# Kernel tuning notes

Measured on AMD Instinct MI355X. Metric: run time of the kernel, lower is better.

The kernel has to match this reference:

```python
import jax, jax.numpy as jnp
import numpy as np

DIM, H, DH = 1024, 16, 64
SCALE = 1.0 / np.sqrt(DH)


def setup_inputs() -> dict:
    key = jax.random.key(0)
    ks = jax.random.split(key, 16)
    B, S = 2, 2048
    glorot = jax.nn.initializers.glorot_uniform()
    def qkv(k):
        return glorot(k, (DIM, H, DH), jnp.float32)
    inp = {
        "x": jax.random.normal(ks[0], (B, S, DIM), jnp.float32),
        "layer_idx": 3,
        "lambda_param": jnp.full((1,), 0.8, jnp.float32),
    }
    for i, br in enumerate(["1", "2"]):
        base = 1 + i * 4
        inp[f"Wq{br}"] = qkv(ks[base])
        inp[f"Wk{br}"] = qkv(ks[base + 1])
        inp[f"Wv{br}"] = qkv(ks[base + 2])
        inp[f"Wo{br}"] = glorot(ks[base + 3], (H, DH, DIM), jnp.float32).reshape(H, DH, DIM)
        inp[f"bq{br}"] = jnp.zeros((H, DH), jnp.float32)
        inp[f"bk{br}"] = jnp.zeros((H, DH), jnp.float32)
        inp[f"bv{br}"] = jnp.zeros((H, DH), jnp.float32)
        inp[f"bo{br}"] = jnp.zeros((DIM,), jnp.float32)
    inp["Wp"] = glorot(ks[9], (DIM, DIM), jnp.float32)
    inp["bp"] = jnp.zeros((DIM,), jnp.float32)
    return inp


def _mha(x, Wq, bq, Wk, bk, Wv, bv, Wo, bo):
    # x: [B,S,D]; per-head projections as in keras.layers.MultiHeadAttention
    q = jnp.einsum("bsd,dhk->bshk", x, Wq) + bq   # [B,S,H,Dh]
    k = jnp.einsum("bsd,dhk->bshk", x, Wk) + bk
    v = jnp.einsum("bsd,dhk->bshk", x, Wv) + bv
    scores = jnp.einsum("bqhd,bkhd->bhqk", q, k) * SCALE  # [B,H,S,S]
    attn = jax.nn.softmax(scores, axis=-1)
    o = jnp.einsum("bhqk,bkhd->bqhd", attn, v)            # [B,S,H,Dh]
    return jnp.einsum("bqhd,hdo->bqo", o, Wo) + bo        # [B,S,D]


def _get_lambda(lambda_param, layer_idx):
    lf = jnp.asarray(layer_idx, jnp.float32)
    exp_term = jnp.exp(-0.3 * jnp.maximum(lf - 1.0, 0.0))
    init = 0.8 - 0.6 * exp_term
    return jnp.clip(init * lambda_param[0], 0.1, 0.9)


def reference(x, layer_idx, lambda_param,
              Wq1, bq1, Wk1, bk1, Wv1, bv1, Wo1, bo1,
              Wq2, bq2, Wk2, bk2, Wv2, bv2, Wo2, bo2,
              Wp, bp):
    a1 = _mha(x, Wq1, bq1, Wk1, bk1, Wv1, bv1, Wo1, bo1)
    a2 = _mha(x, Wq2, bq2, Wk2, bk2, Wv2, bv2, Wo2, bo2)
    lam = _get_lambda(lambda_param, layer_idx)
    diff = a1 - lam * a2
    return diff @ Wp + bp  # dropout is identity at inference
```

## Files before the change

### kernel.cpp

```cpp
#include <hip/hip_runtime.h>
#include <math.h>

typedef unsigned short u16;
typedef __attribute__((ext_vector_type(8))) short bf16x8;
typedef __attribute__((ext_vector_type(4))) float f32x4;
typedef __attribute__((ext_vector_type(4))) unsigned short u16x4;
typedef __attribute__((ext_vector_type(8))) unsigned short u16x8;

constexpr int Sq = 2048, Dm = 1024, Hh = 16, DH = 64;
constexpr int NT = 4096;
constexpr float SEXP = 0.125f * 1.44269504f;

#if __has_builtin(__builtin_amdgcn_exp2f)
#define EXP2(x) __builtin_amdgcn_exp2f(x)
#else
#define EXP2(x) exp2f(x)
#endif

__device__ __forceinline__ u16 f2bf(float f) {
    unsigned u = __float_as_uint(f);
    return (u16)((u + 0x7FFF + ((u >> 16) & 1)) >> 16);
}

__device__ __forceinline__ void async16(u16* lds, const u16* g) {
    __builtin_amdgcn_global_load_lds(
        (const __attribute__((address_space(1))) unsigned int*)g,
        (__attribute__((address_space(3))) unsigned int*)lds, 16, 0, 0);
}

__device__ __forceinline__ float lam_of(const int* lidx, const float* lamp) {
    float lf = (float)lidx[0];
    float init = 0.8f - 0.6f * __expf(-0.3f * fmaxf(lf - 1.0f, 0.0f));
    return fminf(fmaxf(init * lamp[0], 0.1f), 0.9f);
}

__device__ __forceinline__ void gemm_tile_128(
    const u16* __restrict__ A, const u16* __restrict__ Bt, int K,
    int aRow0, int bCol0, u16* As, u16* Bs, f32x4 acc[4][4])
{
    const int tid = threadIdx.x;
    const int w = tid >> 6, lane = tid & 63;
    const int ln = lane & 15, quad = lane >> 4;
    const int wm = (w >> 1) * 64, wn = (w & 1) * 64;
    const int l3 = lane & 7, lr8 = lane >> 3;

    for (int kt = 0; kt < K; kt += 64) {
        __syncthreads();
        #pragma unroll
        for (int c0 = 0; c0 < 4; ++c0) {
            int c = w * 4 + c0;
            int lr = c * 8 + lr8;
            int sc = l3 ^ (lr & 7);
            async16(As + c * 512, A + (size_t)(aRow0 + lr) * K + kt + sc * 8);
            async16(Bs + c * 512, Bt + (size_t)(bCol0 + lr) * K + kt + sc * 8);
        }
        __syncthreads();
        #pragma unroll
        for (int kc = 0; kc < 2; ++kc) {
            bf16x8 af[4], bfr[4];
            #pragma unroll
            for (int mt = 0; mt < 4; ++mt)
                af[mt] = *(const bf16x8*)(As + (wm + mt * 16 + ln) * 64 +
                                          (((kc * 4 + quad) ^ (ln & 7)) * 8));
            #pragma unroll
            for (int nt = 0; nt < 4; ++nt)
                bfr[nt] = *(const bf16x8*)(Bs + (wn + nt * 16 + ln) * 64 +
                                           (((kc * 4 + quad) ^ (ln & 7)) * 8));
            #pragma unroll
            for (int mt = 0; mt < 4; ++mt)
                #pragma unroll
                for (int nt = 0; nt < 4; ++nt)
                    acc[mt][nt] = __builtin_amdgcn_mfma_f32_16x16x32_bf16(
                        af[mt], bfr[nt], acc[mt][nt], 0, 0, 0);
        }
    }
}

__device__ __forceinline__ void gemm_tile_64(
    const u16* __restrict__ A, const u16* __restrict__ Bt, int K,
    int aRow0, int bCol0, u16* As, u16* Bs, f32x4 acc[2][4])
{
    const int tid = threadIdx.x;
    const int w = tid >> 6, lane = tid & 63;
    const int ln = lane & 15, quad = lane >> 4;
    const int wm = (w >> 1) * 32, wn = (w & 1) * 64;
    const int l3 = lane & 7, lr8 = lane >> 3;

    for (int kt = 0; kt < K; kt += 64) {
        __syncthreads();
        #pragma unroll
        for (int c0 = 0; c0 < 2; ++c0) {
            int c = w * 2 + c0;
            int lr = c * 8 + lr8;
            int sc = l3 ^ (lr & 7);
            async16(As + c * 512, A + (size_t)(aRow0 + lr) * K + kt + sc * 8);
        }
        #pragma unroll
        for (int c0 = 0; c0 < 4; ++c0) {
            int c = w * 4 + c0;
            int lr = c * 8 + lr8;
            int sc = l3 ^ (lr & 7);
            async16(Bs + c * 512, Bt + (size_t)(bCol0 + lr) * K + kt + sc * 8);
        }
        __syncthreads();
        #pragma unroll
        for (int kc = 0; kc < 2; ++kc) {
            bf16x8 af[2], bfr[4];
            #pragma unroll
            for (int mt = 0; mt < 2; ++mt)
                af[mt] = *(const bf16x8*)(As + (wm + mt * 16 + ln) * 64 +
                                          (((kc * 4 + quad) ^ (ln & 7)) * 8));
            #pragma unroll
            for (int nt = 0; nt < 4; ++nt)
                bfr[nt] = *(const bf16x8*)(Bs + (wn + nt * 16 + ln) * 64 +
                                           (((kc * 4 + quad) ^ (ln & 7)) * 8));
            #pragma unroll
            for (int mt = 0; mt < 2; ++mt)
                #pragma unroll
                for (int nt = 0; nt < 4; ++nt)
                    acc[mt][nt] = __builtin_amdgcn_mfma_f32_16x16x32_bf16(
                        af[mt], bfr[nt], acc[mt][nt], 0, 0, 0);
        }
    }
}

__global__ __launch_bounds__(256)
void convert_x(const float* __restrict__ x, u16* __restrict__ xb)
{
    int i = (blockIdx.x * 256 + threadIdx.x) * 4;
    float4 v = *(const float4*)(x + i);
    u16x4 o;
    o.x = f2bf(v.x); o.y = f2bf(v.y); o.z = f2bf(v.z); o.w = f2bf(v.w);
    *(u16x4*)(xb + i) = o;
}

struct TcP { const float* src[7]; u16* dst[7]; };

__global__ __launch_bounds__(256)
void wconv(TcP p)
{
    __shared__ float t[64][65];
    const int z = blockIdx.z;
    const float* __restrict__ src = p.src[z];
    u16* __restrict__ dst = p.dst[z];
    const int kb = blockIdx.y * 64, nb = blockIdx.x * 64;
    const int tid = threadIdx.x;
    {
        int r = tid >> 2, cs = (tid & 3) * 16;
        #pragma unroll
        for (int j4 = 0; j4 < 16; j4 += 4) {
            float4 v = *(const float4*)&src[(size_t)(kb + r) * 1024 + nb + cs + j4];
            t[r][cs + j4 + 0] = v.x; t[r][cs + j4 + 1] = v.y;
            t[r][cs + j4 + 2] = v.z; t[r][cs + j4 + 3] = v.w;
        }
    }
    __syncthreads();
    {
        int n = tid >> 2, ks = (tid & 3) * 16;
        u16x8 a, b;
        #pragma unroll
        for (int j = 0; j < 8; ++j) a[j] = f2bf(t[ks + j][n]);
        #pragma unroll
        for (int j = 0; j < 8; ++j) b[j] = f2bf(t[ks + 8 + j][n]);
        u16* o = &dst[(size_t)(nb + n) * 1024 + kb + ks];
        *(u16x8*)o = a;
        *(u16x8*)(o + 8) = b;
    }
}

__global__ __launch_bounds__(256)
void woconv(const float* __restrict__ Wo1, const float* __restrict__ Wo2,
            const float* __restrict__ bo1, const float* __restrict__ bo2,
            const int* __restrict__ lidx, const float* __restrict__ lamp,
            u16* __restrict__ Acat)
{
    const float lam = lam_of(lidx, lamp);
    int i = (blockIdx.x * 256 + threadIdx.x) * 4;
    float4 v;
    if (i < 1048576) {
        v = *(const float4*)(Wo1 + i);
    } else if (i < 2097152) {
        v = *(const float4*)(Wo2 + (i - 1048576));
        v.x *= -lam; v.y *= -lam; v.z *= -lam; v.w *= -lam;
    } else {
        int c = i - 2097152;
        float4 a = *(const float4*)(bo1 + c);
        float4 b = *(const float4*)(bo2 + c);
        v.x = a.x - lam * b.x; v.y = a.y - lam * b.y;
        v.z = a.z - lam * b.z; v.w = a.w - lam * b.w;
    }
    u16x4 o;
    o.x = f2bf(v.x); o.y = f2bf(v.y); o.z = f2bf(v.z); o.w = f2bf(v.w);
    *(u16x4*)(Acat + i) = o;
}

__global__ __launch_bounds__(256, 4)
void wfull_mfma(const u16* __restrict__ Acat, const u16* __restrict__ Wpt,
                const float* __restrict__ bp, u16* __restrict__ Wfull_bt,
                float* __restrict__ bfull)
{
    __shared__ u16 As[64 * 64], Bs[128 * 64];
    const int aRow0 = blockIdx.y * 64, nCol0 = blockIdx.x * 128;
    f32x4 acc[2][4] = {};
    gemm_tile_64(Acat, Wpt, 1024, aRow0, nCol0, As, Bs, acc);

    const int tid = threadIdx.x, w = tid >> 6, lane = tid & 63;
    const int ln = lane & 15, quad = lane >> 4;
    const int wm = (w >> 1) * 32, wn = (w & 1) * 64;
    #pragma unroll
    for (int mt = 0; mt < 2; ++mt) {
        #pragma unroll
        for (int nt = 0; nt < 4; ++nt) {
            int gn = nCol0 + wn + nt * 16 + ln;
            #pragma unroll
            for (int r = 0; r < 4; ++r) {
                int gm = aRow0 + wm + mt * 16 + quad * 4 + r;
                if (gm < 2048)
                    Wfull_bt[(size_t)gn * 2048 + gm] = f2bf(acc[mt][nt][r]);
                else if (gm == 2048)
                    bfull[gn] = acc[mt][nt][r] + bp[gn];
            }
        }
    }
}

struct QkvP { const u16* Wt[6]; const float* bias[6]; u16* out[6]; };

__global__ __launch_bounds__(256, 3)
void qkv_mfma(const u16* __restrict__ xb, QkvP p)
{
    __shared__ u16 As[128 * 64], Bs[128 * 64];
    const int z = blockIdx.z;
    const int type = (z < 3) ? z : z - 3;
    const int aRow0 = blockIdx.y * 128, nCol0 = blockIdx.x * 128;
    f32x4 acc[4][4] = {};
    gemm_tile_128(xb, p.Wt[z], 1024, aRow0, nCol0, As, Bs, acc);

    const float* __restrict__ bias = p.bias[z];
    u16* __restrict__ out = p.out[z];
    const int tid = threadIdx.x, w = tid >> 6, lane = tid & 63;
    const int ln = lane & 15, quad = lane >> 4;
    const int wm = (w >> 1) * 64, wn = (w & 1) * 64;
    #pragma unroll
    for (int mt = 0; mt < 4; ++mt) {
        #pragma unroll
        for (int nt = 0; nt < 4; ++nt) {
            int gn = nCol0 + wn + nt * 16 + ln;
            int h = gn >> 6, dh = gn & 63;
            float bv = bias[gn];
            #pragma unroll
            for (int r = 0; r < 4; ++r) {
                int gm = aRow0 + wm + mt * 16 + quad * 4 + r;
                int b = gm >> 11, s = gm & (Sq - 1);
                size_t bh = (size_t)(b * Hh + h);
                float fv = acc[mt][nt][r] + bv;
                size_t idx;
                u16 val;
                if (type == 0) {
                    val = f2bf(fv * SEXP);
                    idx = bh * 131072 + (size_t)s * 64 + dh;
                } else if (type == 1) {
                    val = f2bf(fv);
                    idx = bh * 131072 + (size_t)(s >> 5) * 2048 +
                          (size_t)((dh >> 5) * 2 + ((s >> 4) & 1)) * 512 +
                          (size_t)(((dh >> 3) & 3) * 16 + (s & 15)) * 8 + (dh & 7);
                } else {
                    val = f2bf(fv);
                    int kidx = ((s & 15) * 2) + ((s >> 4) & 1);
                    idx = bh * 131072 + (size_t)(s >> 5) * 2048 +
                          (size_t)(dh >> 4) * 512 +
                          (size_t)((kidx >> 3) * 16 + (dh & 15)) * 8 + (kidx & 7);
                }
                out[idx] = val;
            }
        }
    }
}

__global__ __launch_bounds__(256, 4)
void attn_mfma(const u16* __restrict__ q1, const u16* __restrict__ kf1,
               const u16* __restrict__ vf1,
               const u16* __restrict__ q2, const u16* __restrict__ kf2,
               const u16* __restrict__ vf2, u16* __restrict__ ocat)
{
    __shared__ __align__(16) char smem[10240];

    const int bh = blockIdx.x, qblk = blockIdx.y, br = blockIdx.z;
    const u16* __restrict__ q  = br ? q2  : q1;
    const u16* __restrict__ kf = br ? kf2 : kf1;
    const u16* __restrict__ vf = br ? vf2 : vf1;

    const int tid = threadIdx.x, w = tid >> 6, lane = tid & 63;
    const int ln = lane & 15, quad = lane >> 4;
    char* Pbase = smem + w * 2560;

    const u16* qbase = q + (size_t)bh * 131072 +
                       (size_t)(qblk * 128 + w * 32) * 64;
    bf16x8 qf[2][2];
    #pragma unroll
    for (int mt = 0; mt < 2; ++mt)
        #pragma unroll
        for (int kc = 0; kc < 2; ++kc)
            qf[mt][kc] = *(const bf16x8*)(qbase + (mt * 16 + ln) * 64 +
                                          kc * 32 + quad * 8);

    bf16x8 ones;
    #pragma unroll
    for (int j = 0; j < 8; ++j) ones[j] = (short)0x3F80;
    const f32x4 zero4 = {0.f, 0.f, 0.f, 0.f};

    f32x4 oacc[2][4] = {};
    f32x4 lacc[2] = {};

    const u16* kbase = kf + (size_t)bh * 131072 + lane * 8;
    const u16* vbase = vf + (size_t)bh * 131072 + lane * 8;

    for (int it = 0; it < 32; ++it) {
        #pragma unroll
        for (int u = 0; u < 2; ++u) {
            const int kt = it * 2 + u;
            const u16* kp = kbase + (size_t)kt * 2048;
            const u16* vp = vbase + (size_t)kt * 2048;

            bf16x8 kfr[2][2];
            #pragma unroll
            for (int kc = 0; kc < 2; ++kc)
                #pragma unroll
                for (int nt = 0; nt < 2; ++nt)
                    kfr[nt][kc] = *(const bf16x8*)(kp + (kc * 2 + nt) * 512);

            f32x4 sacc[2][2];
            #pragma unroll
            for (int mt = 0; mt < 2; ++mt)
                #pragma unroll
                for (int nt = 0; nt < 2; ++nt)
                    sacc[mt][nt] = __builtin_amdgcn_mfma_f32_16x16x32_bf16(
                        qf[mt][0], kfr[nt][0], zero4, 0, 0, 0);
            #pragma unroll
            for (int mt = 0; mt < 2; ++mt)
                #pragma unroll
                for (int nt = 0; nt < 2; ++nt)
                    sacc[mt][nt] = __builtin_amdgcn_mfma_f32_16x16x32_bf16(
                        qf[mt][1], kfr[nt][1], sacc[mt][nt], 0, 0, 0);

            #pragma unroll
            for (int mt = 0; mt < 2; ++mt) {
                #pragma unroll
                for (int r = 0; r < 4; ++r) {
                    float p0 = EXP2(sacc[mt][0][r]);
                    float p1 = EXP2(sacc[mt][1][r]);
                    unsigned a  = __float_as_uint(p0) + 0x8000u;
                    unsigned b2 = __float_as_uint(p1) + 0x8000u;
                    unsigned pk = __builtin_amdgcn_perm(b2, a, 0x07060302);
                    int row = mt * 16 + quad * 4 + r;
                    *(unsigned*)(Pbase + row * 80 + (((ln >> 2) ^ r) << 4) +
                                 ((ln & 3) << 2)) = pk;
                }
            }

            bf16x8 vfr[4];
            #pragma unroll
            for (int dt = 0; dt < 4; ++dt)
                vfr[dt] = *(const bf16x8*)(vp + dt * 512);

            #pragma unroll
            for (int mt = 0; mt < 2; ++mt) {
                bf16x8 pf = *(const bf16x8*)(Pbase + (mt * 16 + ln) * 80 +
                                             ((quad ^ (ln & 3)) << 4));
                lacc[mt] = __builtin_amdgcn_mfma_f32_16x16x32_bf16(
                    pf, ones, lacc[mt], 0, 0, 0);
                #pragma unroll
                for (int dt = 0; dt < 4; ++dt)
                    oacc[mt][dt] = __builtin_amdgcn_mfma_f32_16x16x32_bf16(
                        pf, vfr[dt], oacc[mt][dt], 0, 0, 0);
            }
        }
        __builtin_amdgcn_s_barrier();
    }

    const int b = bh >> 4, h = bh & 15;
    #pragma unroll
    for (int mt = 0; mt < 2; ++mt) {
        #pragma unroll
        for (int r = 0; r < 4; ++r) {
            float inv = 1.0f / lacc[mt][r];
            int s = qblk * 128 + w * 32 + mt * 16 + quad * 4 + r;
            size_t rowb = (size_t)(b * Sq + s) * 2048 + br * 1024 + h * 64;
            #pragma unroll
            for (int dt = 0; dt < 4; ++dt)
                ocat[rowb + dt * 16 + ln] = f2bf(oacc[mt][dt][r] * inv);
        }
    }
}

__global__ __launch_bounds__(256, 4)
void out_mfma(const u16* __restrict__ ocat, const u16* __restrict__ Wfull_bt,
              const float* __restrict__ bfull, float* __restrict__ outb)
{
    __shared__ u16 As[64 * 64], Bs[128 * 64];
    const int aRow0 = blockIdx.y * 64, nCol0 = blockIdx.x * 128;
    f32x4 acc[2][4] = {};
    gemm_tile_64(ocat, Wfull_bt, 2048, aRow0, nCol0, As, Bs, acc);

    const int tid = threadIdx.x, w = tid >> 6, lane = tid & 63;
    const int ln = lane & 15, quad = lane >> 4;
    const int wm = (w >> 1) * 32, wn = (w & 1) * 64;
    #pragma unroll
    for (int mt = 0; mt < 2; ++mt) {
        #pragma unroll
        for (int nt = 0; nt < 4; ++nt) {
            int gn = nCol0 + wn + nt * 16 + ln;
            float bv = bfull[gn];
            #pragma unroll
            for (int r = 0; r < 4; ++r) {
                int gm = aRow0 + wm + mt * 16 + quad * 4 + r;
                outb[(size_t)gm * 1024 + gn] = acc[mt][nt][r] + bv;
            }
        }
    }
}

extern "C" void kernel_launch(void* const* d_in, const int* in_sizes, int n_in,
                              void* d_out, int out_size, void* d_ws, size_t ws_size,
                              hipStream_t stream)
{
    const float* x    = (const float*)d_in[0];
    const int*   lidx = (const int*)  d_in[1];
    const float* lamp = (const float*)d_in[2];
    const float* Wq1  = (const float*)d_in[3];
    const float* Wk1  = (const float*)d_in[4];
    const float* Wv1  = (const float*)d_in[5];
    const float* Wo1  = (const float*)d_in[6];
    const float* bq1  = (const float*)d_in[7];
    const float* bk1  = (const float*)d_in[8];
    const float* bv1  = (const float*)d_in[9];
    const float* bo1  = (const float*)d_in[10];
    const float* Wq2  = (const float*)d_in[11];
    const float* Wk2  = (const float*)d_in[12];
    const float* Wv2  = (const float*)d_in[13];
    const float* Wo2  = (const float*)d_in[14];
    const float* bq2  = (const float*)d_in[15];
    const float* bk2  = (const float*)d_in[16];
    const float* bv2  = (const float*)d_in[17];
    const float* bo2  = (const float*)d_in[18];
    const float* Wp   = (const float*)d_in[19];
    const float* bp   = (const float*)d_in[20];

    char* wsb = (char*)d_ws;
    const size_t MB = 1 << 20;
    u16* xb    = (u16*)(wsb + 0 * MB);
    u16* Wt0   = (u16*)(wsb + 8 * MB);
    u16* Wpt   = (u16*)(wsb + 20 * MB);
    u16* Acat  = (u16*)(wsb + 22 * MB);
    u16* Wfull = (u16*)(wsb + 27 * MB);
    float* bfull = (float*)(wsb + 31 * MB);
    u16* qb1   = (u16*)(wsb + 32 * MB);
    u16* kb1   = (u16*)(wsb + 40 * MB);
    u16* vb1   = (u16*)(wsb + 48 * MB);
    u16* qb2   = (u16*)(wsb + 56 * MB);
    u16* kb2   = (u16*)(wsb + 64 * MB);
    u16* vb2   = (u16*)(wsb + 72 * MB);
    u16* ocat  = (u16*)(wsb + 80 * MB);

    convert_x<<<dim3(NT * Dm / 1024), dim3(256), 0, stream>>>(x, xb);

    TcP tp;
    const float* wsrc[7] = {Wq1, Wk1, Wv1, Wq2, Wk2, Wv2, Wp};
    for (int i = 0; i < 7; ++i) tp.src[i] = wsrc[i];
    for (int i = 0; i < 6; ++i) tp.dst[i] = Wt0 + (size_t)i * 1024 * 1024;
    tp.dst[6] = Wpt;
    wconv<<<dim3(16, 16, 7), dim3(256), 0, stream>>>(tp);

    woconv<<<dim3(2049), dim3(256), 0, stream>>>(
        Wo1, Wo2, bo1, bo2, lidx, lamp, Acat);

    wfull_mfma<<<dim3(8, 33), dim3(256), 0, stream>>>(
        Acat, Wpt, bp, Wfull, bfull);

    QkvP qp;
    qp.Wt[0] = Wt0 + 0 * 1048576; qp.bias[0] = bq1; qp.out[0] = qb1;
    qp.Wt[1] = Wt0 + 1 * 1048576; qp.bias[1] = bk1; qp.out[1] = kb1;
    qp.Wt[2] = Wt0 + 2 * 1048576; qp.bias[2] = bv1; qp.out[2] = vb1;
    qp.Wt[3] = Wt0 + 3 * 1048576; qp.bias[3] = bq2; qp.out[3] = qb2;
    qp.Wt[4] = Wt0 + 4 * 1048576; qp.bias[4] = bk2; qp.out[4] = kb2;
    qp.Wt[5] = Wt0 + 5 * 1048576; qp.bias[5] = bv2; qp.out[5] = vb2;
    qkv_mfma<<<dim3(8, 32, 6), dim3(256), 0, stream>>>(xb, qp);

    attn_mfma<<<dim3(32, 16, 2), dim3(256), 0, stream>>>(
        qb1, kb1, vb1, qb2, kb2, vb2, ocat);

    out_mfma<<<dim3(8, 64), dim3(256), 0, stream>>>(
        ocat, Wfull, bfull, (float*)d_out);
}
```

Baseline: 330.5 us.

## Double-buffer LDS tiles in GEMM helpers to overlap loads with MFMA

```diff
diff --git a/kernel.cpp b/kernel.cpp
--- a/kernel.cpp
+++ b/kernel.cpp
@@ -44,27 +44,43 @@
     const int wm = (w >> 1) * 64, wn = (w & 1) * 64;
     const int l3 = lane & 7, lr8 = lane >> 3;
 
+    #pragma unroll
+    for (int c0 = 0; c0 < 4; ++c0) {
+        int c = w * 4 + c0;
+        int lr = c * 8 + lr8;
+        int sc = l3 ^ (lr & 7);
+        async16(As + c * 512, A + (size_t)(aRow0 + lr) * K + sc * 8);
+        async16(Bs + c * 512, Bt + (size_t)(bCol0 + lr) * K + sc * 8);
+    }
+    __syncthreads();
+
+    int cur = 0;
     for (int kt = 0; kt < K; kt += 64) {
-        __syncthreads();
-        #pragma unroll
-        for (int c0 = 0; c0 < 4; ++c0) {
-            int c = w * 4 + c0;
-            int lr = c * 8 + lr8;
-            int sc = l3 ^ (lr & 7);
-            async16(As + c * 512, A + (size_t)(aRow0 + lr) * K + kt + sc * 8);
-            async16(Bs + c * 512, Bt + (size_t)(bCol0 + lr) * K + kt + sc * 8);
-        }
-        __syncthreads();
+        const int ktn = kt + 64;
+        if (ktn < K) {
+            u16* Asn = As + (cur ^ 1) * 8192;
+            u16* Bsn = Bs + (cur ^ 1) * 8192;
+            #pragma unroll
+            for (int c0 = 0; c0 < 4; ++c0) {
+                int c = w * 4 + c0;
+                int lr = c * 8 + lr8;
+                int sc = l3 ^ (lr & 7);
+                async16(Asn + c * 512, A + (size_t)(aRow0 + lr) * K + ktn + sc * 8);
+                async16(Bsn + c * 512, Bt + (size_t)(bCol0 + lr) * K + ktn + sc * 8);
+            }
+        }
+        const u16* Asc = As + cur * 8192;
+        const u16* Bsc = Bs + cur * 8192;
         #pragma unroll
         for (int kc = 0; kc < 2; ++kc) {
             bf16x8 af[4], bfr[4];
             #pragma unroll
             for (int mt = 0; mt < 4; ++mt)
-                af[mt] = *(const bf16x8*)(As + (wm + mt * 16 + ln) * 64 +
+                af[mt] = *(const bf16x8*)(Asc + (wm + mt * 16 + ln) * 64 +
                                           (((kc * 4 + quad) ^ (ln & 7)) * 8));
             #pragma unroll
             for (int nt = 0; nt < 4; ++nt)
-                bfr[nt] = *(const bf16x8*)(Bs + (wn + nt * 16 + ln) * 64 +
+                bfr[nt] = *(const bf16x8*)(Bsc + (wn + nt * 16 + ln) * 64 +
                                            (((kc * 4 + quad) ^ (ln & 7)) * 8));
             #pragma unroll
             for (int mt = 0; mt < 4; ++mt)
@@ -73,6 +89,8 @@
                     acc[mt][nt] = __builtin_amdgcn_mfma_f32_16x16x32_bf16(
                         af[mt], bfr[nt], acc[mt][nt], 0, 0, 0);
         }
+        __syncthreads();
+        cur ^= 1;
     }
 }
 
@@ -86,33 +104,55 @@
     const int wm = (w >> 1) * 32, wn = (w & 1) * 64;
     const int l3 = lane & 7, lr8 = lane >> 3;
 
+    #pragma unroll
+    for (int c0 = 0; c0 < 2; ++c0) {
+        int c = w * 2 + c0;
+        int lr = c * 8 + lr8;
+        int sc = l3 ^ (lr & 7);
+        async16(As + c * 512, A + (size_t)(aRow0 + lr) * K + sc * 8);
+    }
+    #pragma unroll
+    for (int c0 = 0; c0 < 4; ++c0) {
+        int c = w * 4 + c0;
+        int lr = c * 8 + lr8;
+        int sc = l3 ^ (lr & 7);
+        async16(Bs + c * 512, Bt + (size_t)(bCol0 + lr) * K + sc * 8);
+    }
+    __syncthreads();
+
+    int cur = 0;
     for (int kt = 0; kt < K; kt += 64) {
-        __syncthreads();
-        #pragma unroll
-        for (int c0 = 0; c0 < 2; ++c0) {
-            int c = w * 2 + c0;
-            int lr = c * 8 + lr8;
-            int sc = l3 ^ (lr & 7);
-            async16(As + c * 512, A + (size_t)(aRow0 + lr) * K + kt + sc * 8);
-        }
-        #pragma unroll
-        for (int c0 = 0; c0 < 4; ++c0) {
-            int c = w * 4 + c0;
-            int lr = c * 8 + lr8;
-            int sc = l3 ^ (lr & 7);
-            async16(Bs + c * 512, Bt + (size_t)(bCol0 + lr) * K + kt + sc * 8);
-        }
-        __syncthreads();
+        const int ktn = kt + 64;
+        if (ktn < K) {
+            u16* Asn = As + (cur ^ 1) * 4096;
+            u16* Bsn = Bs + (cur ^ 1) * 8192;
+            #pragma unroll
+            for (int c0 = 0; c0 < 2; ++c0) {
+                int c = w * 2 + c0;
+                int lr = c * 8 + lr8;
+                int sc = l3 ^ (lr & 7);
+                async16(Asn + c * 512, A + (size_t)(aRow0 + lr) * K + ktn + sc * 8);
+            }
+            #pragma unroll
+            for (int c0 = 0; c0 < 4; ++c0) {
+                int c = w * 4 + c0;
+                int lr = c * 8 + lr8;
+                int sc = l3 ^ (lr & 7);
+                async16(Bsn + c * 512, Bt + (size_t)(bCol0 + lr) * K + ktn + sc * 8);
+            }
+        }
+        const u16* Asc = As + cur * 4096;
+        const u16* Bsc = Bs + cur * 8192;
         #pragma unroll
         for (int kc = 0; kc < 2; ++kc) {
             bf16x8 af[2], bfr[4];
             #pragma unroll
             for (int mt = 0; mt < 2; ++mt)
-                af[mt] = *(const bf16x8*)(As + (wm + mt * 16 + ln) * 64 +
+                af[mt] = *(const bf16x8*)(Asc + (wm + mt * 16 + ln) * 64 +
                                           (((kc * 4 + quad) ^ (ln & 7)) * 8));
             #pragma unroll
             for (int nt = 0; nt < 4; ++nt)
-                bfr[nt] = *(const bf16x8*)(Bs + (wn + nt * 16 + ln) * 64 +
+                bfr[nt] = *(const bf16x8*)(Bsc + (wn + nt * 16 + ln) * 64 +
                                            (((kc * 4 + quad) ^ (ln & 7)) * 8));
             #pragma unroll
             for (int mt = 0; mt < 2; ++mt)
@@ -121,6 +161,8 @@
                     acc[mt][nt] = __builtin_amdgcn_mfma_f32_16x16x32_bf16(
                         af[mt], bfr[nt], acc[mt][nt], 0, 0, 0);
         }
+        __syncthreads();
+        cur ^= 1;
     }
 }
 
@@ -194,12 +236,12 @@
     *(u16x4*)(Acat + i) = o;
 }
 
-__global__ __launch_bounds__(256, 4)
+__global__ __launch_bounds__(256, 3)
 void wfull_mfma(const u16* __restrict__ Acat, const u16* __restrict__ Wpt,
                 const float* __restrict__ bp, u16* __restrict__ Wfull_bt,
                 float* __restrict__ bfull)
 {
-    __shared__ u16 As[64 * 64], Bs[128 * 64];
+    __shared__ u16 As[2 * 4096], Bs[2 * 8192];
     const int aRow0 = blockIdx.y * 64, nCol0 = blockIdx.x * 128;
     f32x4 acc[2][4] = {};
     gemm_tile_64(Acat, Wpt, 1024, aRow0, nCol0, As, Bs, acc);
@@ -226,10 +268,10 @@
 
 struct QkvP { const u16* Wt[6]; const float* bias[6]; u16* out[6]; };
 
-__global__ __launch_bounds__(256, 3)
+__global__ __launch_bounds__(256, 2)
 void qkv_mfma(const u16* __restrict__ xb, QkvP p)
 {
-    __shared__ u16 As[128 * 64], Bs[128 * 64];
+    __shared__ u16 As[2 * 8192], Bs[2 * 8192];
     const int z = blockIdx.z;
     const int type = (z < 3) ? z : z - 3;
     const int aRow0 = blockIdx.y * 128, nCol0 = blockIdx.x * 128;
@@ -393,11 +435,11 @@
     }
 }
 
-__global__ __launch_bounds__(256, 4)
+__global__ __launch_bounds__(256, 3)
 void out_mfma(const u16* __restrict__ ocat, const u16* __restrict__ Wfull_bt,
               const float* __restrict__ bfull, float* __restrict__ outb)
 {
-    __shared__ u16 As[64 * 64], Bs[128 * 64];
+    __shared__ u16 As[2 * 4096], Bs[2 * 8192];
     const int aRow0 = blockIdx.y * 64, nCol0 = blockIdx.x * 128;
     f32x4 acc[2][4] = {};
     gemm_tile_64(ocat, Wfull_bt, 2048, aRow0, nCol0, As, Bs, acc);
```

After: 344.1 us. 4.1% more time.
